# Kernel tuning notes

Measured on AMD Instinct MI355X. Metric: run time of the kernel, lower is better.

## Reference

```python
import jax, jax.numpy as jnp
import numpy as np

EPS = 1e-3  # Keras LayerNormalization default epsilon


def _layer_norm(x, gamma, beta):
    mu = jnp.mean(x, axis=-1, keepdims=True)
    var = jnp.mean(jnp.square(x - mu), axis=-1, keepdims=True)
    return (x - mu) * jax.lax.rsqrt(var + EPS) * gamma + beta


def setup_inputs() -> dict:
    key = jax.random.key(0)
    ks = jax.random.split(key, 8)
    B, T, E = 4, 4096, 1024
    s = 1.0 / np.sqrt(E)
    return {
        "token": jax.random.normal(ks[0], (B, T, E), dtype=jnp.float32),
        "Wk": jax.random.normal(ks[1], (E, 1), dtype=jnp.float32) * s,
        "bk": jnp.zeros((1,), dtype=jnp.float32),
        "Wq": jax.random.normal(ks[2], (E, 1), dtype=jnp.float32) * s,
        "bq": jnp.zeros((1,), dtype=jnp.float32),
        "Wv": jax.random.normal(ks[3], (E, E), dtype=jnp.float32) * s,
        "bv": jnp.zeros((E,), dtype=jnp.float32),
        "gamma1": jnp.ones((E,), dtype=jnp.float32),
        "beta1": jnp.zeros((E,), dtype=jnp.float32),
        "gamma2": jnp.ones((E,), dtype=jnp.float32),
        "beta2": jnp.zeros((E,), dtype=jnp.float32),
    }


def reference(token, Wk, bk, Wq, bq, Wv, bv, gamma1, beta1, gamma2, beta2):
    # scalar key/query per token: Dense(1) then drop the trailing unit dim
    key = (token @ Wk + bk)[:, :, 0]      # [B,T]
    query = (token @ Wq + bq)[:, :, 0]    # [B,T]
    value = token @ Wv + bv               # [B,T,E]
    # rank-1 outer-product scores, softmax over key axis
    kq = jnp.einsum('bt,bx->btx', query, key)   # [B,T,T]
    index = jax.nn.softmax(kq, axis=2)
    z = jnp.einsum('btx,bxe->bte', index, value)  # [B,T,E]
    z = _layer_norm(z, gamma1, beta1)
    z = _layer_norm((z @ Wv + bv) + z, gamma2, beta2)
    return jax.nn.relu(z)
```

## Files before the change

### kernel.cpp

```cpp
#include <hip/hip_runtime.h>
#include <cstdint>
#include <cstddef>

#define B_ 4
#define T_ 4096
#define E_ 1024
#define BT_ (B_*T_)
#define G_ 128
#define SK_ 16

typedef unsigned short u16;
typedef unsigned int   u32;
typedef __attribute__((ext_vector_type(8))) short bf8;
typedef __attribute__((ext_vector_type(4))) float f4;

__device__ inline u16 f2bf(float f){
  u32 x = __float_as_uint(f);
  u32 r = (x + 0x7fffu + ((x >> 16) & 1u)) >> 16;
  return (u16)r;
}
__device__ inline float bf2f(u32 u){ return __uint_as_float(u << 16); }

__device__ inline float wredsum(float v){
  #pragma unroll
  for (int o = 32; o; o >>= 1) v += __shfl_xor(v, o, 64);
  return v;
}

__device__ inline float hw_exp2(float x){
#if __has_builtin(__builtin_amdgcn_exp2f)
  return __builtin_amdgcn_exp2f(x);
#else
  return exp2f(x);
#endif
}

__device__ inline void gld_lds16(const void* g, void* l){
  __builtin_amdgcn_global_load_lds(
      (const __attribute__((address_space(1))) void*)g,
      (__attribute__((address_space(3))) void*)l, 16, 0, 0);
}

#define LOG2E_ 1.44269504088896340f

#define NB_TOKT_ 4096
#define NB_WVT_  1024
__global__ __launch_bounds__(256) void k_pre(const float* __restrict__ token,
    const float* __restrict__ Wk, const float* __restrict__ bk,
    const float* __restrict__ Wq, const float* __restrict__ bq,
    const float* __restrict__ Wv,
    u16* __restrict__ tokT, u16* __restrict__ wvT,
    float* __restrict__ key, float* __restrict__ query){
  __shared__ u16 tile2[64][66];
  int bid = blockIdx.x;
  int tid = threadIdx.x;
  if (bid < NB_TOKT_){
    int xt = bid & 63, et = (bid >> 6) & 15, b = bid >> 10;
    const float* ib = token + (size_t)b * T_ * E_;
    u16*         ob = tokT  + (size_t)b * E_ * T_;
    int tx = tid & 63, ty0 = tid >> 6;
    #pragma unroll
    for (int p = 0; p < 16; ++p){
      int ty = ty0 + p*4;
      tile2[ty][tx] = f2bf(ib[(size_t)(xt*64+ty)*E_ + et*64 + tx]);
    }
    __syncthreads();
    int e  = tid >> 4;
    int t4 = (tid & 15) * 4;
    #pragma unroll
    for (int p = 0; p < 4; ++p){
      int ee = e + p*16;
      u16 v0 = tile2[t4+0][ee];
      u16 v1 = tile2[t4+1][ee];
      u16 v2 = tile2[t4+2][ee];
      u16 v3 = tile2[t4+3][ee];
      uint2 pk;
      pk.x = (u32)v0 | ((u32)v1 << 16);
      pk.y = (u32)v2 | ((u32)v3 << 16);
      *(uint2*)(ob + (size_t)(et*64+ee)*T_ + xt*64 + t4) = pk;
    }
  } else if (bid < NB_TOKT_ + NB_WVT_){
    u16 (*tile)[33] = (u16(*)[33])tile2;
    int idx = bid - NB_TOKT_;
    int nt = idx & 31, kt = idx >> 5;
    int tx = tid & 31, ty0 = tid >> 5;
    #pragma unroll
    for (int p = 0; p < 4; ++p){
      int ty = ty0 + p*8;
      tile[ty][tx] = f2bf(Wv[(size_t)(kt*32+ty)*E_ + nt*32 + tx]);
    }
    __syncthreads();
    #pragma unroll
    for (int p = 0; p < 4; ++p){
      int ty = ty0 + p*8;
      wvT[(size_t)(nt*32+ty)*E_ + kt*32 + tx] = tile[tx][ty];
    }
  } else {
    int rg   = bid - (NB_TOKT_ + NB_WVT_);
    int row  = rg * 4 + (tid >> 6);
    int lane = tid & 63;
    const f4* tr = (const f4*)(token + (size_t)row * E_);
    const f4* wk = (const f4*)Wk;
    const f4* wq = (const f4*)Wq;
    float sk = 0.f, sq = 0.f;
    #pragma unroll
    for (int it = 0; it < 4; ++it){
      f4 t = tr[lane + 64*it];
      f4 a = wk[lane + 64*it];
      f4 b = wq[lane + 64*it];
      sk += t.x*a.x + t.y*a.y + t.z*a.z + t.w*a.w;
      sq += t.x*b.x + t.y*b.y + t.z*b.z + t.w*b.w;
    }
    sk = wredsum(sk); sq = wredsum(sq);
    if (lane == 0){ key[row] = sk + bk[0]; query[row] = sq + bq[0]; }
  }
}

__global__ __launch_bounds__(256) void k_pgen(const float* __restrict__ key,
    const float* __restrict__ query, float* __restrict__ kstat,
    u16* __restrict__ P, float* __restrict__ dnode){
  __shared__ float shred[32];
  int r = blockIdx.x;
  int b = r >> 7;
  int i = r & (G_-1);
  int tid = threadIdx.x, lane = tid & 63, w = tid >> 6;
  const f4* kb = (const f4*)(key   + (size_t)b * T_);
  const f4* qb = (const f4*)(query + (size_t)b * T_);
  f4 kv[4];
  float kmx = -3.4e38f, kmn = 3.4e38f, qmx = -3.4e38f, qmn = 3.4e38f;
  #pragma unroll
  for (int it = 0; it < 4; ++it){
    kv[it] = kb[tid + it*256];
    kmx = fmaxf(kmx, fmaxf(fmaxf(kv[it].x, kv[it].y), fmaxf(kv[it].z, kv[it].w)));
    kmn = fminf(kmn, fminf(fminf(kv[it].x, kv[it].y), fminf(kv[it].z, kv[it].w)));
    f4 qv = qb[tid + it*256];
    qmx = fmaxf(qmx, fmaxf(fmaxf(qv.x, qv.y), fmaxf(qv.z, qv.w)));
    qmn = fminf(qmn, fminf(fminf(qv.x, qv.y), fminf(qv.z, qv.w)));
  }
  #pragma unroll
  for (int o = 32; o; o >>= 1){
    kmx = fmaxf(kmx, __shfl_xor(kmx, o, 64));
    kmn = fminf(kmn, __shfl_xor(kmn, o, 64));
    qmx = fmaxf(qmx, __shfl_xor(qmx, o, 64));
    qmn = fminf(qmn, __shfl_xor(qmn, o, 64));
  }
  if (lane == 0){
    shred[w*4+0] = kmx; shred[w*4+1] = kmn;
    shred[w*4+2] = qmx; shred[w*4+3] = qmn;
  }
  __syncthreads();
  if (tid == 0){
    shred[16] = fmaxf(fmaxf(shred[0], shred[4]),  fmaxf(shred[8],  shred[12]));
    shred[17] = fminf(fminf(shred[1], shred[5]),  fminf(shred[9],  shred[13]));
    shred[18] = fmaxf(fmaxf(shred[2], shred[6]),  fmaxf(shred[10], shred[14]));
    shred[19] = fminf(fminf(shred[3], shred[7]),  fminf(shred[11], shred[15]));
  }
  __syncthreads();
  kmx = shred[16]; kmn = shred[17]; qmx = shred[18]; qmn = shred[19];
  if (i == 0 && tid == 0){
    kstat[b*4+0] = kmx; kstat[b*4+1] = kmn;
    kstat[b*4+2] = qmx; kstat[b*4+3] = qmn;
  }
  float g = qmn + (qmx - qmn) * ((float)i * (1.f/(G_-1)));
  float m = (g > 0.f) ? g*kmx : g*kmn;
  float gL = g * LOG2E_, mL = m * LOG2E_;
  u16* pr = P + (size_t)r * T_;
  float s = 0.f;
  #pragma unroll
  for (int it = 0; it < 4; ++it){
    int idx = tid + it*256;
    u16 e0 = f2bf(hw_exp2(gL*kv[it].x - mL));
    u16 e1 = f2bf(hw_exp2(gL*kv[it].y - mL));
    u16 e2 = f2bf(hw_exp2(gL*kv[it].z - mL));
    u16 e3 = f2bf(hw_exp2(gL*kv[it].w - mL));
    s += bf2f(e0) + bf2f(e1) + bf2f(e2) + bf2f(e3);
    uint2 pk;
    pk.x = (u32)e0 | ((u32)e1 << 16);
    pk.y = (u32)e2 | ((u32)e3 << 16);
    *(uint2*)(pr + (size_t)idx*4) = pk;
  }
  s = wredsum(s);
  __syncthreads();
  if (lane == 0) shred[20 + w] = s;
  __syncthreads();
  if (tid == 0) dnode[r] = shred[20] + shred[21] + shred[22] + shred[23];
}

__global__ __launch_bounds__(256) void k_cgemm(const u16* __restrict__ A,
    const u16* __restrict__ Bt, const float* __restrict__ dnode,
    u16* __restrict__ C){
  __shared__ __align__(16) u16 lA[128*32];
  __shared__ __align__(16) u16 lB[128*32];
  const int K = T_;
  int bid = blockIdx.x;
  int xcd = bid & 7;
  int j   = bid >> 3;
  int cc  = xcd + 8*(j >> 3);
  int b   = cc >> 4, ks = cc & (SK_-1);
  int n0  = (j & 7) * 128;
  int m0  = b*G_;
  const u16* Bp = Bt + (size_t)b * E_ * T_;
  int k_beg = ks * (T_/SK_);
  int tid = threadIdx.x, lane = tid & 63, w = tid >> 6;
  int wr = w >> 1, wc = w & 1, h = lane >> 4, l15 = lane & 15;
  f4 acc[4][4] = {};
  for (int ki = 0; ki < T_/SK_; ki += 32){
    int k0 = k_beg + ki;
    __syncthreads();
    #pragma unroll
    for (int p = 0; p < 2; ++p){
      int u = p*256 + w*64 + lane;
      int row = u >> 2;
      int sl  = (u & 3) ^ ((row >> 1) & 3);
      const u16* ga = A  + (size_t)(m0 + row) * K + k0 + sl*8;
      const u16* gb = Bp + (size_t)(n0 + row) * K + k0 + sl*8;
      gld_lds16(ga, lA + (size_t)(p*256 + w*64)*8);
      gld_lds16(gb, lB + (size_t)(p*256 + w*64)*8);
    }
    __syncthreads();
    bf8 a[4], bfr[4];
    #pragma unroll
    for (int f = 0; f < 4; ++f){
      int ra = wr*64 + f*16 + l15;
      int rb = wc*64 + f*16 + l15;
      a[f]   = *(const bf8*)&lA[ra*32 + ((h ^ ((ra >> 1) & 3)) & 3)*8];
      bfr[f] = *(const bf8*)&lB[rb*32 + ((h ^ ((rb >> 1) & 3)) & 3)*8];
    }
    #pragma unroll
    for (int fm = 0; fm < 4; ++fm)
    #pragma unroll
    for (int fn = 0; fn < 4; ++fn)
      acc[fm][fn] = __builtin_amdgcn_mfma_f32_16x16x32_bf16(a[fm], bfr[fn], acc[fm][fn], 0,0,0);
  }
  u16* Ch = C + (size_t)ks * (B_*G_) * E_;
  #pragma unroll
  for (int fm = 0; fm < 4; ++fm)
  #pragma unroll
  for (int r = 0; r < 4; ++r){
    int row = m0 + wr*64 + fm*16 + h*4 + r;
    float inv = 1.f / dnode[row];
    #pragma unroll
    for (int fn = 0; fn < 4; ++fn){
      int col = n0 + wc*64 + fn*16 + l15;
      Ch[(size_t)row * E_ + col] = f2bf(acc[fm][fn][r] * inv);
    }
  }
}

__global__ __launch_bounds__(256) void k_csum(const u16* __restrict__ C,
                                              u16* __restrict__ Cn){
  size_t idx = ((size_t)blockIdx.x * 256 + threadIdx.x) * 8;
  const size_t H = (size_t)(B_*G_) * E_;
  float s[8] = {};
  #pragma unroll
  for (int q = 0; q < SK_; ++q){
    uint4 v = *(const uint4*)(C + q*H + idx);
    u32 u[4] = {v.x, v.y, v.z, v.w};
    #pragma unroll
    for (int jv = 0; jv < 4; ++jv){
      s[2*jv]   += bf2f(u[jv] & 0xffffu);
      s[2*jv+1] += bf2f(u[jv] >> 16);
    }
  }
  uint4 pk;
  pk.x = (u32)f2bf(s[0]) | ((u32)f2bf(s[1]) << 16);
  pk.y = (u32)f2bf(s[2]) | ((u32)f2bf(s[3]) << 16);
  pk.z = (u32)f2bf(s[4]) | ((u32)f2bf(s[5]) << 16);
  pk.w = (u32)f2bf(s[6]) | ((u32)f2bf(s[7]) << 16);
  *(uint4*)(Cn + idx) = pk;
}

__global__ __launch_bounds__(256) void k_ngemm(const u16* __restrict__ A,
    const u16* __restrict__ Bt, float* __restrict__ P){
  __shared__ __align__(16) u16 lA[128*32];
  __shared__ __align__(16) u16 lB[128*32];
  const int K = E_, N = E_;
  int bid = blockIdx.x;
  int ks  = bid >> 5;
  int r   = bid & 31;
  int n0  = (r & 7) * 128;
  int m0  = (r >> 3) * 128;
  int k_beg = ks * (K/SK_);
  int tid = threadIdx.x, lane = tid & 63, w = tid >> 6;
  int wr = w >> 1, wc = w & 1, h = lane >> 4, l15 = lane & 15;
  f4 acc[4][4] = {};
  for (int ki = 0; ki < K/SK_; ki += 32){
    int k0 = k_beg + ki;
    __syncthreads();
    #pragma unroll
    for (int p = 0; p < 2; ++p){
      int u = p*256 + w*64 + lane;
      int row = u >> 2;
      int sl  = (u & 3) ^ ((row >> 1) & 3);
      const u16* ga = A  + (size_t)(m0 + row) * K + k0 + sl*8;
      const u16* gb = Bt + (size_t)(n0 + row) * K + k0 + sl*8;
      gld_lds16(ga, lA + (size_t)(p*256 + w*64)*8);
      gld_lds16(gb, lB + (size_t)(p*256 + w*64)*8);
    }
    __syncthreads();
    bf8 a[4], bfr[4];
    #pragma unroll
    for (int f = 0; f < 4; ++f){
      int ra = wr*64 + f*16 + l15;
      int rb = wc*64 + f*16 + l15;
      a[f]   = *(const bf8*)&lA[ra*32 + ((h ^ ((ra >> 1) & 3)) & 3)*8];
      bfr[f] = *(const bf8*)&lB[rb*32 + ((h ^ ((rb >> 1) & 3)) & 3)*8];
    }
    #pragma unroll
    for (int fm = 0; fm < 4; ++fm)
    #pragma unroll
    for (int fn = 0; fn < 4; ++fn)
      acc[fm][fn] = __builtin_amdgcn_mfma_f32_16x16x32_bf16(a[fm], bfr[fn], acc[fm][fn], 0,0,0);
  }
  float* Ph = P + (size_t)ks * (B_*G_) * E_;
  #pragma unroll
  for (int fm = 0; fm < 4; ++fm)
  #pragma unroll
  for (int rr = 0; rr < 4; ++rr){
    int row = m0 + wr*64 + fm*16 + h*4 + rr;
    #pragma unroll
    for (int fn = 0; fn < 4; ++fn){
      int col = n0 + wc*64 + fn*16 + l15;
      Ph[(size_t)row * N + col] = acc[fm][fn][rr];
    }
  }
}

__global__ __launch_bounds__(256) void k_combln1(const float* __restrict__ P,
    const float* __restrict__ bias,
    const float* __restrict__ g, const float* __restrict__ bt,
    u16* __restrict__ z1){
  const size_t Hq = (size_t)(B_*G_) * E_;
  int row  = blockIdx.x * 4 + (threadIdx.x >> 6);
  int lane = threadIdx.x & 63;
  const f4* A0 = (const f4*)(P + (size_t)row * E_) + lane*4;
  const f4* gb = (const f4*)bias + lane*4;
  float v[16];
  #pragma unroll
  for (int jj = 0; jj < 4; ++jj){
    f4 z = gb[jj];
    v[4*jj+0] = z.x; v[4*jj+1] = z.y; v[4*jj+2] = z.z; v[4*jj+3] = z.w;
  }
  #pragma unroll
  for (int q = 0; q < SK_; ++q){
    const f4* Aq = A0 + q*(Hq/4);
    #pragma unroll
    for (int jj = 0; jj < 4; ++jj){
      f4 x = Aq[jj];
      v[4*jj+0] += x.x; v[4*jj+1] += x.y; v[4*jj+2] += x.z; v[4*jj+3] += x.w;
    }
  }
  float s1 = 0.f, s2 = 0.f;
  #pragma unroll
  for (int j = 0; j < 16; ++j){ s1 += v[j]; s2 += v[j]*v[j]; }
  s1 = wredsum(s1); s2 = wredsum(s2);
  float mean = s1 * (1.f/E_);
  float var  = s2 * (1.f/E_) - mean*mean;
  float rs   = rsqrtf(var + 1e-3f);
  const f4* g4 = (const f4*)g + lane*4;
  const f4* b4 = (const f4*)bt + lane*4;
  u16* ob = z1 + (size_t)row * E_ + lane*16;
  u32 pu[8];
  #pragma unroll
  for (int jj = 0; jj < 4; ++jj){
    f4 gg = g4[jj], bb = b4[jj];
    float o0 = (v[4*jj+0]-mean)*rs*gg.x + bb.x;
    float o1 = (v[4*jj+1]-mean)*rs*gg.y + bb.y;
    float o2 = (v[4*jj+2]-mean)*rs*gg.z + bb.z;
    float o3 = (v[4*jj+3]-mean)*rs*gg.w + bb.w;
    pu[2*jj]   = (u32)f2bf(o0) | ((u32)f2bf(o1) << 16);
    pu[2*jj+1] = (u32)f2bf(o2) | ((u32)f2bf(o3) << 16);
  }
  uint4 w0 = {pu[0], pu[1], pu[2], pu[3]};
  uint4 w1 = {pu[4], pu[5], pu[6], pu[7]};
  *(uint4*)ob       = w0;
  *(uint4*)(ob + 8) = w1;
}

__global__ __launch_bounds__(256) void k_combln2(const float* __restrict__ P,
    const float* __restrict__ bias, const u16* __restrict__ resid,
    const float* __restrict__ g, const float* __restrict__ bt,
    float* __restrict__ Y){
  const size_t Hq = (size_t)(B_*G_) * E_;
  int row  = blockIdx.x * 4 + (threadIdx.x >> 6);
  int lane = threadIdx.x & 63;
  const f4* A0 = (const f4*)(P + (size_t)row * E_) + lane*4;
  const f4* gb = (const f4*)bias + lane*4;
  const u16* rr = resid + (size_t)row * E_ + lane*16;
  uint4 r0 = *(const uint4*)rr;
  uint4 r1 = *(const uint4*)(rr + 8);
  u32 ru[8] = {r0.x, r0.y, r0.z, r0.w, r1.x, r1.y, r1.z, r1.w};
  float v[16];
  #pragma unroll
  for (int jj = 0; jj < 4; ++jj){
    f4 z = gb[jj];
    v[4*jj+0] = z.x + bf2f(ru[2*jj]   & 0xffffu);
    v[4*jj+1] = z.y + bf2f(ru[2*jj]   >> 16);
    v[4*jj+2] = z.z + bf2f(ru[2*jj+1] & 0xffffu);
    v[4*jj+3] = z.w + bf2f(ru[2*jj+1] >> 16);
  }
  #pragma unroll
  for (int q = 0; q < SK_; ++q){
    const f4* Aq = A0 + q*(Hq/4);
    #pragma unroll
    for (int jj = 0; jj < 4; ++jj){
      f4 x = Aq[jj];
      v[4*jj+0] += x.x; v[4*jj+1] += x.y; v[4*jj+2] += x.z; v[4*jj+3] += x.w;
    }
  }
  float s1 = 0.f, s2 = 0.f;
  #pragma unroll
  for (int j = 0; j < 16; ++j){ s1 += v[j]; s2 += v[j]*v[j]; }
  s1 = wredsum(s1); s2 = wredsum(s2);
  float mean = s1 * (1.f/E_);
  float var  = s2 * (1.f/E_) - mean*mean;
  float rs   = rsqrtf(var + 1e-3f);
  const f4* g4 = (const f4*)g + lane*4;
  const f4* b4 = (const f4*)bt + lane*4;
  f4* od = (f4*)(Y + (size_t)row * E_ + lane*16);
  #pragma unroll
  for (int jj = 0; jj < 4; ++jj){
    f4 gg = g4[jj], bb = b4[jj];
    f4 t;
    t.x = (v[4*jj+0]-mean)*rs*gg.x + bb.x;
    t.y = (v[4*jj+1]-mean)*rs*gg.y + bb.y;
    t.z = (v[4*jj+2]-mean)*rs*gg.z + bb.z;
    t.w = (v[4*jj+3]-mean)*rs*gg.w + bb.w;
    od[jj] = t;
  }
}

__global__ __launch_bounds__(256) void k_interp(const float* __restrict__ query,
    const float* __restrict__ kstat, const float* __restrict__ Y,
    float* __restrict__ outp){
  int row  = blockIdx.x * 4 + (threadIdx.x >> 6);
  int lane = threadIdx.x & 63;
  int b = row >> 12;
  float qmax = kstat[b*4+2], qmin = kstat[b*4+3];
  float q = query[row];
  float u = (q - qmin) * ((float)(G_-1) / (qmax - qmin));
  int i = (int)u;
  if (i < 0) i = 0;
  if (i > G_-2) i = G_-2;
  float a = fminf(fmaxf(u - (float)i, 0.f), 1.f);
  const f4* Y0 = (const f4*)(Y + ((size_t)(b*G_ + i)) * E_) + lane*4;
  const f4* Y1 = Y0 + (E_/4);
  f4* od = (f4*)(outp + (size_t)row * E_ + lane*16);
  #pragma unroll
  for (int jj = 0; jj < 4; ++jj){
    f4 x0 = Y0[jj], x1 = Y1[jj];
    f4 t;
    t.x = fmaxf(x0.x + a*(x1.x - x0.x), 0.f);
    t.y = fmaxf(x0.y + a*(x1.y - x0.y), 0.f);
    t.z = fmaxf(x0.z + a*(x1.z - x0.z), 0.f);
    t.w = fmaxf(x0.w + a*(x1.w - x0.w), 0.f);
    od[jj] = t;
  }
}

extern "C" void kernel_launch(void* const* d_in, const int* in_sizes, int n_in,
                              void* d_out, int out_size, void* d_ws, size_t ws_size,
                              hipStream_t stream){
  const float* token = (const float*)d_in[0];
  const float* Wk    = (const float*)d_in[1];
  const float* bk    = (const float*)d_in[2];
  const float* Wq    = (const float*)d_in[3];
  const float* bq    = (const float*)d_in[4];
  const float* Wv    = (const float*)d_in[5];
  const float* bv    = (const float*)d_in[6];
  const float* g1    = (const float*)d_in[7];
  const float* b1    = (const float*)d_in[8];
  const float* g2    = (const float*)d_in[9];
  const float* b2    = (const float*)d_in[10];

  char* ws = (char*)d_ws;
  u16*   wvT   = (u16*)ws;
  float* key   = (float*)(ws + (2u<<20));
  float* query = (float*)(ws + (2u<<20) + (64u<<10));
  float* dnode = (float*)(ws + (2u<<20) + (128u<<10));
  float* kstat = (float*)(ws + (2u<<20) + (256u<<10));
  u16*   X      = (u16*)(ws + (4u<<20));
  u16*   V      = (u16*)(ws + (36u<<20));
  u16*   Pp     = X;
  float* Ynode  = (float*)X;
  u16*   tokT   = V;
  u16*   Cn     = V;
  u16*   z1node = (u16*)(ws + (36u<<20) + (8u<<20));
  u16*   Cq  = (u16*)d_out;
  float* Pf  = (float*)d_out;
  float* out = (float*)d_out;

  k_pre  <<<dim3(NB_TOKT_ + NB_WVT_ + BT_/4), 256, 0, stream>>>(
      token, Wk, bk, Wq, bq, Wv, tokT, wvT, key, query);
  k_pgen <<<dim3(B_*G_), 256, 0, stream>>>(key, query, kstat, Pp, dnode);
  k_cgemm<<<dim3(512), 256, 0, stream>>>(Pp, tokT, dnode, Cq);
  k_csum <<<dim3((B_*G_)*E_/(256*8)), 256, 0, stream>>>(Cq, Cn);
  k_ngemm<<<dim3(512), 256, 0, stream>>>(Cn, wvT, Pf);
  k_combln1<<<dim3(B_*G_/4), 256, 0, stream>>>(Pf, bv, g1, b1, z1node);
  k_ngemm<<<dim3(512), 256, 0, stream>>>(z1node, wvT, Pf);
  k_combln2<<<dim3(B_*G_/4), 256, 0, stream>>>(Pf, bv, z1node, g2, b2, Ynode);
  k_interp<<<dim3(BT_/4), 256, 0, stream>>>(query, kstat, Ynode, out);
}
```

Baseline: 126.3 us.

## Fuse softmax probability generation into chunk GEMM and normalization into split-K sum

Removes the separate probability-generation kernel. The chunk GEMM now computes the bf16 exp weights in registers from key and per-node query slopes, so the P matrix is no longer written to or read from global memory and only the token tile is staged in LDS. The per-node softmax denominators move into the split-K reduction kernel, which applies the normalization after summing. In exchange, every GEMM block recomputes the key/query min/max reductions and its exponentials, and the reduction kernel now does 2x4096 exps per block.

```diff
diff --git a/kernel.cpp b/kernel.cpp
--- a/kernel.cpp
+++ b/kernel.cpp
@@ -13,6 +13,8 @@
 typedef unsigned int   u32;
 typedef __attribute__((ext_vector_type(8))) short bf8;
 typedef __attribute__((ext_vector_type(4))) float f4;
+
+union punAB { uint4 u; bf8 v; };
 
 __device__ inline u16 f2bf(float f){
   u32 x = __float_as_uint(f);
@@ -116,81 +118,11 @@
   }
 }
 
-__global__ __launch_bounds__(256) void k_pgen(const float* __restrict__ key,
-    const float* __restrict__ query, float* __restrict__ kstat,
-    u16* __restrict__ P, float* __restrict__ dnode){
-  __shared__ float shred[32];
-  int r = blockIdx.x;
-  int b = r >> 7;
-  int i = r & (G_-1);
-  int tid = threadIdx.x, lane = tid & 63, w = tid >> 6;
-  const f4* kb = (const f4*)(key   + (size_t)b * T_);
-  const f4* qb = (const f4*)(query + (size_t)b * T_);
-  f4 kv[4];
-  float kmx = -3.4e38f, kmn = 3.4e38f, qmx = -3.4e38f, qmn = 3.4e38f;
-  #pragma unroll
-  for (int it = 0; it < 4; ++it){
-    kv[it] = kb[tid + it*256];
-    kmx = fmaxf(kmx, fmaxf(fmaxf(kv[it].x, kv[it].y), fmaxf(kv[it].z, kv[it].w)));
-    kmn = fminf(kmn, fminf(fminf(kv[it].x, kv[it].y), fminf(kv[it].z, kv[it].w)));
-    f4 qv = qb[tid + it*256];
-    qmx = fmaxf(qmx, fmaxf(fmaxf(qv.x, qv.y), fmaxf(qv.z, qv.w)));
-    qmn = fminf(qmn, fminf(fminf(qv.x, qv.y), fminf(qv.z, qv.w)));
-  }
-  #pragma unroll
-  for (int o = 32; o; o >>= 1){
-    kmx = fmaxf(kmx, __shfl_xor(kmx, o, 64));
-    kmn = fminf(kmn, __shfl_xor(kmn, o, 64));
-    qmx = fmaxf(qmx, __shfl_xor(qmx, o, 64));
-    qmn = fminf(qmn, __shfl_xor(qmn, o, 64));
-  }
-  if (lane == 0){
-    shred[w*4+0] = kmx; shred[w*4+1] = kmn;
-    shred[w*4+2] = qmx; shred[w*4+3] = qmn;
-  }
-  __syncthreads();
-  if (tid == 0){
-    shred[16] = fmaxf(fmaxf(shred[0], shred[4]),  fmaxf(shred[8],  shred[12]));
-    shred[17] = fminf(fminf(shred[1], shred[5]),  fminf(shred[9],  shred[13]));
-    shred[18] = fmaxf(fmaxf(shred[2], shred[6]),  fmaxf(shred[10], shred[14]));
-    shred[19] = fminf(fminf(shred[3], shred[7]),  fminf(shred[11], shred[15]));
-  }
-  __syncthreads();
-  kmx = shred[16]; kmn = shred[17]; qmx = shred[18]; qmn = shred[19];
-  if (i == 0 && tid == 0){
-    kstat[b*4+0] = kmx; kstat[b*4+1] = kmn;
-    kstat[b*4+2] = qmx; kstat[b*4+3] = qmn;
-  }
-  float g = qmn + (qmx - qmn) * ((float)i * (1.f/(G_-1)));
-  float m = (g > 0.f) ? g*kmx : g*kmn;
-  float gL = g * LOG2E_, mL = m * LOG2E_;
-  u16* pr = P + (size_t)r * T_;
-  float s = 0.f;
-  #pragma unroll
-  for (int it = 0; it < 4; ++it){
-    int idx = tid + it*256;
-    u16 e0 = f2bf(hw_exp2(gL*kv[it].x - mL));
-    u16 e1 = f2bf(hw_exp2(gL*kv[it].y - mL));
-    u16 e2 = f2bf(hw_exp2(gL*kv[it].z - mL));
-    u16 e3 = f2bf(hw_exp2(gL*kv[it].w - mL));
-    s += bf2f(e0) + bf2f(e1) + bf2f(e2) + bf2f(e3);
-    uint2 pk;
-    pk.x = (u32)e0 | ((u32)e1 << 16);
-    pk.y = (u32)e2 | ((u32)e3 << 16);
-    *(uint2*)(pr + (size_t)idx*4) = pk;
-  }
-  s = wredsum(s);
-  __syncthreads();
-  if (lane == 0) shred[20 + w] = s;
-  __syncthreads();
-  if (tid == 0) dnode[r] = shred[20] + shred[21] + shred[22] + shred[23];
-}
-
-__global__ __launch_bounds__(256) void k_cgemm(const u16* __restrict__ A,
-    const u16* __restrict__ Bt, const float* __restrict__ dnode,
+__global__ __launch_bounds__(256) void k_cgemm(const float* __restrict__ key,
+    const float* __restrict__ query, const u16* __restrict__ Bt,
     u16* __restrict__ C){
-  __shared__ __align__(16) u16 lA[128*32];
   __shared__ __align__(16) u16 lB[128*32];
+  __shared__ float shred[20];
   const int K = T_;
   int bid = blockIdx.x;
   int xcd = bid & 7;
@@ -198,11 +130,55 @@
   int cc  = xcd + 8*(j >> 3);
   int b   = cc >> 4, ks = cc & (SK_-1);
   int n0  = (j & 7) * 128;
-  int m0  = b*G_;
   const u16* Bp = Bt + (size_t)b * E_ * T_;
   int k_beg = ks * (T_/SK_);
   int tid = threadIdx.x, lane = tid & 63, w = tid >> 6;
   int wr = w >> 1, wc = w & 1, h = lane >> 4, l15 = lane & 15;
+
+  const f4* kb4 = (const f4*)(key   + (size_t)b * T_);
+  const f4* qb4 = (const f4*)(query + (size_t)b * T_);
+  float kmx = -3.4e38f, kmn = 3.4e38f, qmx = -3.4e38f, qmn = 3.4e38f;
+  #pragma unroll
+  for (int it = 0; it < 4; ++it){
+    f4 kv = kb4[tid + it*256];
+    kmx = fmaxf(kmx, fmaxf(fmaxf(kv.x, kv.y), fmaxf(kv.z, kv.w)));
+    kmn = fminf(kmn, fminf(fminf(kv.x, kv.y), fminf(kv.z, kv.w)));
+    f4 qv = qb4[tid + it*256];
+    qmx = fmaxf(qmx, fmaxf(fmaxf(qv.x, qv.y), fmaxf(qv.z, qv.w)));
+    qmn = fminf(qmn, fminf(fminf(qv.x, qv.y), fminf(qv.z, qv.w)));
+  }
+  #pragma unroll
+  for (int o = 32; o; o >>= 1){
+    kmx = fmaxf(kmx, __shfl_xor(kmx, o, 64));
+    kmn = fminf(kmn, __shfl_xor(kmn, o, 64));
+    qmx = fmaxf(qmx, __shfl_xor(qmx, o, 64));
+    qmn = fminf(qmn, __shfl_xor(qmn, o, 64));
+  }
+  if (lane == 0){
+    shred[w*4+0] = kmx; shred[w*4+1] = kmn;
+    shred[w*4+2] = qmx; shred[w*4+3] = qmn;
+  }
+  __syncthreads();
+  if (tid == 0){
+    shred[16] = fmaxf(fmaxf(shred[0], shred[4]),  fmaxf(shred[8],  shred[12]));
+    shred[17] = fminf(fminf(shred[1], shred[5]),  fminf(shred[9],  shred[13]));
+    shred[18] = fmaxf(fmaxf(shred[2], shred[6]),  fmaxf(shred[10], shred[14]));
+    shred[19] = fminf(fminf(shred[3], shred[7]),  fminf(shred[11], shred[15]));
+  }
+  __syncthreads();
+  kmx = shred[16]; kmn = shred[17]; qmx = shred[18]; qmn = shred[19];
+
+  float gL[4], mL[4];
+  #pragma unroll
+  for (int f = 0; f < 4; ++f){
+    int i = wr*64 + f*16 + l15;
+    float g = qmn + (qmx - qmn) * ((float)i * (1.f/(G_-1)));
+    float m = (g > 0.f) ? g*kmx : g*kmn;
+    gL[f] = g * LOG2E_;
+    mL[f] = m * LOG2E_;
+  }
+  const float* kbp = key + (size_t)b * T_;
+
   f4 acc[4][4] = {};
   for (int ki = 0; ki < T_/SK_; ki += 32){
     int k0 = k_beg + ki;
@@ -212,44 +188,125 @@
       int u = p*256 + w*64 + lane;
       int row = u >> 2;
       int sl  = (u & 3) ^ ((row >> 1) & 3);
-      const u16* ga = A  + (size_t)(m0 + row) * K + k0 + sl*8;
-      const u16* gb = Bp + (size_t)(n0 + row) * K + k0 + sl*8;
-      gld_lds16(ga, lA + (size_t)(p*256 + w*64)*8);
-      gld_lds16(gb, lB + (size_t)(p*256 + w*64)*8);
+      gld_lds16(Bp + (size_t)(n0 + row) * K + k0 + sl*8,
+                lB + (size_t)(p*256 + w*64)*8);
+    }
+    f4 kv0 = *(const f4*)(kbp + k0 + h*8);
+    f4 kv1 = *(const f4*)(kbp + k0 + h*8 + 4);
+    bf8 af[4];
+    #pragma unroll
+    for (int f = 0; f < 4; ++f){
+      u16 e0 = f2bf(hw_exp2(gL[f]*kv0.x - mL[f]));
+      u16 e1 = f2bf(hw_exp2(gL[f]*kv0.y - mL[f]));
+      u16 e2 = f2bf(hw_exp2(gL[f]*kv0.z - mL[f]));
+      u16 e3 = f2bf(hw_exp2(gL[f]*kv0.w - mL[f]));
+      u16 e4 = f2bf(hw_exp2(gL[f]*kv1.x - mL[f]));
+      u16 e5 = f2bf(hw_exp2(gL[f]*kv1.y - mL[f]));
+      u16 e6 = f2bf(hw_exp2(gL[f]*kv1.z - mL[f]));
+      u16 e7 = f2bf(hw_exp2(gL[f]*kv1.w - mL[f]));
+      punAB pa;
+      pa.u.x = (u32)e0 | ((u32)e1 << 16);
+      pa.u.y = (u32)e2 | ((u32)e3 << 16);
+      pa.u.z = (u32)e4 | ((u32)e5 << 16);
+      pa.u.w = (u32)e6 | ((u32)e7 << 16);
+      af[f] = pa.v;
     }
     __syncthreads();
-    bf8 a[4], bfr[4];
+    bf8 bfr[4];
     #pragma unroll
     for (int f = 0; f < 4; ++f){
-      int ra = wr*64 + f*16 + l15;
       int rb = wc*64 + f*16 + l15;
-      a[f]   = *(const bf8*)&lA[ra*32 + ((h ^ ((ra >> 1) & 3)) & 3)*8];
       bfr[f] = *(const bf8*)&lB[rb*32 + ((h ^ ((rb >> 1) & 3)) & 3)*8];
     }
     #pragma unroll
     for (int fm = 0; fm < 4; ++fm)
     #pragma unroll
     for (int fn = 0; fn < 4; ++fn)
-      acc[fm][fn] = __builtin_amdgcn_mfma_f32_16x16x32_bf16(a[fm], bfr[fn], acc[fm][fn], 0,0,0);
+      acc[fm][fn] = __builtin_amdgcn_mfma_f32_16x16x32_bf16(af[fm], bfr[fn], acc[fm][fn], 0,0,0);
   }
   u16* Ch = C + (size_t)ks * (B_*G_) * E_;
+  int m0 = b*G_;
   #pragma unroll
   for (int fm = 0; fm < 4; ++fm)
   #pragma unroll
   for (int r = 0; r < 4; ++r){
     int row = m0 + wr*64 + fm*16 + h*4 + r;
-    float inv = 1.f / dnode[row];
     #pragma unroll
     for (int fn = 0; fn < 4; ++fn){
       int col = n0 + wc*64 + fn*16 + l15;
-      Ch[(size_t)row * E_ + col] = f2bf(acc[fm][fn][r] * inv);
+      Ch[(size_t)row * E_ + col] = f2bf(acc[fm][fn][r]);
     }
   }
 }
 
 __global__ __launch_bounds__(256) void k_csum(const u16* __restrict__ C,
-                                              u16* __restrict__ Cn){
-  size_t idx = ((size_t)blockIdx.x * 256 + threadIdx.x) * 8;
+    const float* __restrict__ key, const float* __restrict__ query,
+    float* __restrict__ kstat, u16* __restrict__ Cn){
+  __shared__ float shred[28];
+  int bid = blockIdx.x, tid = threadIdx.x, lane = tid & 63, w = tid >> 6;
+  int r0 = bid * 2;
+  int b  = r0 >> 7;
+  const f4* kb4 = (const f4*)(key   + (size_t)b * T_);
+  const f4* qb4 = (const f4*)(query + (size_t)b * T_);
+  f4 kv[4];
+  float kmx = -3.4e38f, kmn = 3.4e38f, qmx = -3.4e38f, qmn = 3.4e38f;
+  #pragma unroll
+  for (int it = 0; it < 4; ++it){
+    kv[it] = kb4[tid + it*256];
+    kmx = fmaxf(kmx, fmaxf(fmaxf(kv[it].x, kv[it].y), fmaxf(kv[it].z, kv[it].w)));
+    kmn = fminf(kmn, fminf(fminf(kv[it].x, kv[it].y), fminf(kv[it].z, kv[it].w)));
+    f4 qv = qb4[tid + it*256];
+    qmx = fmaxf(qmx, fmaxf(fmaxf(qv.x, qv.y), fmaxf(qv.z, qv.w)));
+    qmn = fminf(qmn, fminf(fminf(qv.x, qv.y), fminf(qv.z, qv.w)));
+  }
+  #pragma unroll
+  for (int o = 32; o; o >>= 1){
+    kmx = fmaxf(kmx, __shfl_xor(kmx, o, 64));
+    kmn = fminf(kmn, __shfl_xor(kmn, o, 64));
+    qmx = fmaxf(qmx, __shfl_xor(qmx, o, 64));
+    qmn = fminf(qmn, __shfl_xor(qmn, o, 64));
+  }
+  if (lane == 0){
+    shred[w*4+0] = kmx; shred[w*4+1] = kmn;
+    shred[w*4+2] = qmx; shred[w*4+3] = qmn;
+  }
+  __syncthreads();
+  if (tid == 0){
+    shred[16] = fmaxf(fmaxf(shred[0], shred[4]),  fmaxf(shred[8],  shred[12]));
+    shred[17] = fminf(fminf(shred[1], shred[5]),  fminf(shred[9],  shred[13]));
+    shred[18] = fmaxf(fmaxf(shred[2], shred[6]),  fmaxf(shred[10], shred[14]));
+    shred[19] = fminf(fminf(shred[3], shred[7]),  fminf(shred[11], shred[15]));
+  }
+  __syncthreads();
+  kmx = shred[16]; kmn = shred[17]; qmx = shred[18]; qmn = shred[19];
+  if ((r0 & (G_-1)) == 0 && tid == 0){
+    kstat[b*4+0] = kmx; kstat[b*4+1] = kmn;
+    kstat[b*4+2] = qmx; kstat[b*4+3] = qmn;
+  }
+  int i0 = r0 & (G_-1);
+  float ga = qmn + (qmx - qmn) * ((float)i0     * (1.f/(G_-1)));
+  float gb = qmn + (qmx - qmn) * ((float)(i0+1) * (1.f/(G_-1)));
+  float ma = (ga > 0.f) ? ga*kmx : ga*kmn;
+  float mb = (gb > 0.f) ? gb*kmx : gb*kmn;
+  float gaL = ga * LOG2E_, maL = ma * LOG2E_;
+  float gbL = gb * LOG2E_, mbL = mb * LOG2E_;
+  float d0 = 0.f, d1 = 0.f;
+  #pragma unroll
+  for (int it = 0; it < 4; ++it){
+    f4 k4 = kv[it];
+    d0 += bf2f(f2bf(hw_exp2(gaL*k4.x - maL))) + bf2f(f2bf(hw_exp2(gaL*k4.y - maL)))
+        + bf2f(f2bf(hw_exp2(gaL*k4.z - maL))) + bf2f(f2bf(hw_exp2(gaL*k4.w - maL)));
+    d1 += bf2f(f2bf(hw_exp2(gbL*k4.x - mbL))) + bf2f(f2bf(hw_exp2(gbL*k4.y - mbL)))
+        + bf2f(f2bf(hw_exp2(gbL*k4.z - mbL))) + bf2f(f2bf(hw_exp2(gbL*k4.w - mbL)));
+  }
+  d0 = wredsum(d0); d1 = wredsum(d1);
+  __syncthreads();
+  if (lane == 0){ shred[20 + w] = d0; shred[24 + w] = d1; }
+  __syncthreads();
+  float inv0 = 1.f / (shred[20] + shred[21] + shred[22] + shred[23]);
+  float inv1 = 1.f / (shred[24] + shred[25] + shred[26] + shred[27]);
+  float inv = (tid < 128) ? inv0 : inv1;
+  size_t idx = ((size_t)bid * 256 + tid) * 8;
   const size_t H = (size_t)(B_*G_) * E_;
   float s[8] = {};
   #pragma unroll
@@ -263,10 +320,10 @@
     }
   }
   uint4 pk;
-  pk.x = (u32)f2bf(s[0]) | ((u32)f2bf(s[1]) << 16);
-  pk.y = (u32)f2bf(s[2]) | ((u32)f2bf(s[3]) << 16);
-  pk.z = (u32)f2bf(s[4]) | ((u32)f2bf(s[5]) << 16);
-  pk.w = (u32)f2bf(s[6]) | ((u32)f2bf(s[7]) << 16);
+  pk.x = (u32)f2bf(s[0]*inv) | ((u32)f2bf(s[1]*inv) << 16);
+  pk.y = (u32)f2bf(s[2]*inv) | ((u32)f2bf(s[3]*inv) << 16);
+  pk.z = (u32)f2bf(s[4]*inv) | ((u32)f2bf(s[5]*inv) << 16);
+  pk.w = (u32)f2bf(s[6]*inv) | ((u32)f2bf(s[7]*inv) << 16);
   *(uint4*)(Cn + idx) = pk;
 }
 
@@ -477,11 +534,9 @@
   u16*   wvT   = (u16*)ws;
   float* key   = (float*)(ws + (2u<<20));
   float* query = (float*)(ws + (2u<<20) + (64u<<10));
-  float* dnode = (float*)(ws + (2u<<20) + (128u<<10));
   float* kstat = (float*)(ws + (2u<<20) + (256u<<10));
   u16*   X      = (u16*)(ws + (4u<<20));
   u16*   V      = (u16*)(ws + (36u<<20));
-  u16*   Pp     = X;
   float* Ynode  = (float*)X;
   u16*   tokT   = V;
   u16*   Cn     = V;
@@ -492,9 +547,8 @@
 
   k_pre  <<<dim3(NB_TOKT_ + NB_WVT_ + BT_/4), 256, 0, stream>>>(
       token, Wk, bk, Wq, bq, Wv, tokT, wvT, key, query);
-  k_pgen <<<dim3(B_*G_), 256, 0, stream>>>(key, query, kstat, Pp, dnode);
-  k_cgemm<<<dim3(512), 256, 0, stream>>>(Pp, tokT, dnode, Cq);
-  k_csum <<<dim3((B_*G_)*E_/(256*8)), 256, 0, stream>>>(Cq, Cn);
+  k_cgemm<<<dim3(512), 256, 0, stream>>>(key, query, tokT, Cq);
+  k_csum <<<dim3((B_*G_)*E_/(256*8)), 256, 0, stream>>>(Cq, key, query, kstat, Cn);
   k_ngemm<<<dim3(512), 256, 0, stream>>>(Cn, wvT, Pf);
   k_combln1<<<dim3(B_*G_/4), 256, 0, stream>>>(Pf, bv, g1, b1, z1node);
   k_ngemm<<<dim3(512), 256, 0, stream>>>(z1node, wvT, Pf);
```

Result: no change. 128.0 us (+1.3%).
